# Optimization experiments

Hardware: AMD Instinct MI355X
Metric: run time of the kernel (lower is better)

The kernel has to match this reference:

```python
import jax, jax.numpy as jnp
import numpy as np
import math

VOCAB, D, H, NL, L, B = 50257, 768, 12, 4, 1024, 2
DH = D // H
DFF = 4 * D
ALPHA = 0.25
NEG = -1e9


def _ln(x, g, b, eps=1e-5):
    mu = x.mean(-1, keepdims=True)
    var = ((x - mu) ** 2).mean(-1, keepdims=True)
    return (x - mu) * jax.lax.rsqrt(var + eps) * g + b


def setup_inputs() -> dict:
    key = jax.random.key(0)
    ks = jax.random.split(key, 16)
    s = 0.02
    tokens = jax.random.randint(ks[0], (B, L), 0, VOCAB)
    timelike_mask = jax.random.randint(ks[1], (NL, D), 0, 2).astype(jnp.int32)
    embed = jax.random.normal(ks[2], (VOCAB, D), jnp.float32) * s
    pos_emb = jax.random.normal(ks[3], (L, D), jnp.float32) * s
    wq = jax.random.normal(ks[4], (NL, D, D), jnp.float32) * s
    wk = jax.random.normal(ks[5], (NL, D, D), jnp.float32) * s
    wv = jax.random.normal(ks[6], (NL, D, D), jnp.float32) * s
    wo = jax.random.normal(ks[7], (NL, D, D), jnp.float32) * s
    ff_w1 = jax.random.normal(ks[8], (NL, DFF, D), jnp.float32) * s
    ff_b1 = jnp.zeros((NL, DFF), jnp.float32)
    ff_w2 = jax.random.normal(ks[9], (NL, D, DFF), jnp.float32) * s
    ff_b2 = jnp.zeros((NL, D), jnp.float32)
    ln1_g = jnp.ones((NL, D), jnp.float32); ln1_b = jnp.zeros((NL, D), jnp.float32)
    ln2_g = jnp.ones((NL, D), jnp.float32); ln2_b = jnp.zeros((NL, D), jnp.float32)
    lnf_g = jnp.ones((D,), jnp.float32); lnf_b = jnp.zeros((D,), jnp.float32)
    return dict(tokens=tokens, timelike_mask=timelike_mask, embed=embed, pos_emb=pos_emb,
                wq=wq, wk=wk, wv=wv, wo=wo,
                ln1_g=ln1_g, ln1_b=ln1_b, ln2_g=ln2_g, ln2_b=ln2_b,
                ff_w1=ff_w1, ff_b1=ff_b1, ff_w2=ff_w2, ff_b2=ff_b2,
                lnf_g=lnf_g, lnf_b=lnf_b)


def reference(tokens, timelike_mask, embed, pos_emb, wq, wk, wv, wo,
              ln1_g, ln1_b, ln2_g, ln2_b, ff_w1, ff_b1, ff_w2, ff_b2,
              lnf_g, lnf_b):
    Bc, Lc = tokens.shape
    scale = math.sqrt(DH)
    # embeddings: token + learned position
    h = embed[tokens] + pos_emb[None, :Lc]  # (B,L,D)
    # additive causal mask, matching torch's -inf attention_mask convention
    causal = jnp.where(jnp.tril(jnp.ones((Lc, Lc), bool)), 0.0, NEG)[None, None]  # (1,1,L,L)
    for i in range(NL):
        xn = _ln(h, ln1_g[i], ln1_b[i])
        # nn.Linear(bias=False): y = x @ W.T, W is (out,in)
        q = jnp.einsum('bld,od->blo', xn, wq[i]).reshape(Bc, Lc, H, DH).astype(jnp.float32)
        k = jnp.einsum('bld,od->blo', xn, wk[i]).reshape(Bc, Lc, H, DH).astype(jnp.float32)
        v = jnp.einsum('bld,od->blo', xn, wv[i]).reshape(Bc, Lc, H, DH)
        # Minkowski term: scores_std - 2*alpha*(Q*P_t)K^T  ==  (Q*(1-2*alpha*m)) K^T
        m = timelike_mask[i].astype(jnp.float32).reshape(H, DH)  # per-head timelike directions
        q_eff = q * (1.0 - 2.0 * ALPHA * m)[None, None]
        scores = jnp.einsum('bqhd,bkhd->bhqk', q_eff, k) / scale + causal
        aw = jax.nn.softmax(scores, axis=-1)  # dropout=0 (eval)
        attn = jnp.einsum('bhqk,bkhd->bqhd', aw, v).reshape(Bc, Lc, D)
        h = h + jnp.einsum('bld,od->blo', attn, wo[i])
        xn2 = _ln(h, ln2_g[i], ln2_b[i])
        ff = jax.nn.gelu(jnp.einsum('bld,fd->blf', xn2, ff_w1[i]) + ff_b1[i], approximate=False)
        h = h + jnp.einsum('blf,df->bld', ff, ff_w2[i]) + ff_b2[i]
    h = _ln(h, lnf_g, lnf_b)
    logits = jnp.einsum('bld,vd->blv', h, embed)  # tied LM head
    return logits
```

## Files before the change

kernel.cpp:

```cpp
#include <hip/hip_runtime.h>
#include <math.h>

#define VOCABSZ 50257
#define VPAD 50432
#define DMODEL 768
#define NHEAD 12
#define NLAYER 4
#define SEQ 1024
#define BATCH 2
#define DHEAD 64
#define DFFN 3072
#define BT (BATCH * SEQ)
#define NBH (BATCH * NHEAD)

typedef __attribute__((ext_vector_type(8))) short bf16x8;
typedef __attribute__((ext_vector_type(4))) float f32x4;

__device__ __forceinline__ ushort f2bf(float f) {
  uint u = __builtin_bit_cast(uint, f);
  u = (u + 0x7fffu + ((u >> 16) & 1u)) >> 16;
  return (ushort)u;
}

__device__ __forceinline__ float bf2f(ushort u) {
  uint x = ((uint)u) << 16;
  return __builtin_bit_cast(float, x);
}

__device__ __forceinline__ void gl_lds16(const ushort* g, ushort* l) {
  __builtin_amdgcn_global_load_lds(
      (const __attribute__((address_space(1))) void*)g,
      (__attribute__((address_space(3))) void*)l, 16, 0, 0);
}

__global__ __launch_bounds__(256) void conv_qkv3_kernel(
    const float* __restrict__ wq, const float* __restrict__ wk,
    const float* __restrict__ wv, ushort* __restrict__ dst) {
  const int per4 = DMODEL * DMODEL / 4;
  const int total = NLAYER * per4;
  int i = blockIdx.x * 256 + threadIdx.x;
  if (i >= 3 * total) return;
  int which = i / total;
  int rem = i - which * total;
  const float* src = (which == 0) ? wq : (which == 1) ? wk : wv;
  int layer = rem / per4, r2 = rem % per4;
  float4 v = reinterpret_cast<const float4*>(src)[rem];
  reinterpret_cast<ushort4*>(dst)[(size_t)layer * (3 * per4) + which * per4 +
                                  r2] =
      make_ushort4(f2bf(v.x), f2bf(v.y), f2bf(v.z), f2bf(v.w));
}

__global__ __launch_bounds__(256) void conv3_kernel(
    const float* __restrict__ wo, ushort* __restrict__ wo_b,
    const float* __restrict__ fw1, ushort* __restrict__ fw1_b,
    const float* __restrict__ fw2, ushort* __restrict__ fw2_b) {
  const int n1 = NLAYER * DMODEL * DMODEL / 4;
  const int nf = NLAYER * DFFN * DMODEL / 4;
  int i = blockIdx.x * 256 + threadIdx.x;
  const float* src;
  ushort* dst;
  int idx;
  if (i < n1) {
    src = wo; dst = wo_b; idx = i;
  } else if (i < n1 + nf) {
    src = fw1; dst = fw1_b; idx = i - n1;
  } else if (i < n1 + 2 * nf) {
    src = fw2; dst = fw2_b; idx = i - n1 - nf;
  } else {
    return;
  }
  float4 v = reinterpret_cast<const float4*>(src)[idx];
  reinterpret_cast<ushort4*>(dst)[idx] =
      make_ushort4(f2bf(v.x), f2bf(v.y), f2bf(v.z), f2bf(v.w));
}

__global__ __launch_bounds__(256) void conv_embed_kernel(
    const float* __restrict__ emb, ushort* __restrict__ dst) {
  int i = blockIdx.x * 256 + threadIdx.x;
  if (i >= VPAD * DMODEL / 4) return;
  int row = (i * 4) / DMODEL;
  ushort4 o = make_ushort4(0, 0, 0, 0);
  if (row < VOCABSZ) {
    float4 v = reinterpret_cast<const float4*>(emb)[i];
    o = make_ushort4(f2bf(v.x), f2bf(v.y), f2bf(v.z), f2bf(v.w));
  }
  reinterpret_cast<ushort4*>(dst)[i] = o;
}

template <int KS, bool RBIAS, bool EMB>
__global__ __launch_bounds__(256) void ln_kernel(
    float* __restrict__ h, const ushort* __restrict__ part,
    const float* __restrict__ rb, const int* __restrict__ tok,
    const float* __restrict__ emb, const float* __restrict__ pos,
    const float* __restrict__ g, const float* __restrict__ bta,
    ushort* __restrict__ o) {
  __shared__ float red[8];
  int row = blockIdx.x;
  int tid = threadIdx.x;
  float* xr = h + (size_t)row * DMODEL;
  const float* er = nullptr;
  const float* pr = nullptr;
  if (EMB) {
    er = emb + (size_t)tok[row] * DMODEL;
    pr = pos + (size_t)(row & (SEQ - 1)) * DMODEL;
  }
  float v[3];
  float s = 0.f, sq = 0.f;
#pragma unroll
  for (int j = 0; j < 3; ++j) {
    int c = tid + j * 256;
    float a;
    if (EMB) {
      a = er[c] + pr[c];
      xr[c] = a;
    } else {
      a = xr[c];
      if (RBIAS) a += rb[c];
      if (KS > 0) {
#pragma unroll
        for (int z = 0; z < KS; ++z)
          a += bf2f(part[(size_t)z * BT * DMODEL + (size_t)row * DMODEL + c]);
        xr[c] = a;
      }
    }
    v[j] = a;
    s += a;
    sq += a * a;
  }
#pragma unroll
  for (int off = 1; off < 64; off <<= 1) {
    s += __shfl_xor(s, off);
    sq += __shfl_xor(sq, off);
  }
  int wid = tid >> 6;
  if ((tid & 63) == 0) { red[wid * 2] = s; red[wid * 2 + 1] = sq; }
  __syncthreads();
  float S = red[0] + red[2] + red[4] + red[6];
  float SQ = red[1] + red[3] + red[5] + red[7];
  float mu = S * (1.0f / DMODEL);
  float var = SQ * (1.0f / DMODEL) - mu * mu;
  float r = rsqrtf(var + 1e-5f);
  ushort* orow = o + (size_t)row * DMODEL;
#pragma unroll
  for (int j = 0; j < 3; ++j) {
    int c = tid + j * 256;
    orow[c] = f2bf((v[j] - mu) * r * g[c] + bta[c]);
  }
}

__global__ __launch_bounds__(256) void fattn_kernel(
    const ushort* __restrict__ q, const ushort* __restrict__ k,
    const ushort* __restrict__ vt, float* __restrict__ Opart,
    float* __restrict__ ml) {
  __shared__ __align__(16) ushort Ks[2][64 * 64];
  __shared__ __align__(16) ushort Vs[2][64 * 64];
  __shared__ __align__(16) ushort Ps[4][16][80];
  const int bid = blockIdx.x;
  const int wgid = (bid & 7) * 96 + (bid >> 3);
  const int z = wgid / 32;
  const int rem = wgid % 32;
  const int qb_ = rem >> 1, s = rem & 1;
  const int b = z / NHEAD, hh = z % NHEAD;
  const int q0 = (15 - qb_) * 64;
  const int tcnt = (q0 >> 6) + 1;
  const int half0 = (tcnt + 1) >> 1;
  const int tbeg = s ? half0 : 0;
  const int tend = s ? tcnt : half0;
  const int tid = threadIdx.x, w = tid >> 6, l = tid & 63;
  const int fr = l & 15, ks = l >> 4;
  const int qrow = q0 + w * 16 + fr;
  const size_t ri = (size_t)z * SEQ + qrow;
  const size_t R = (size_t)NBH * SEQ;
  const size_t off = (s ? R : 0) + ri;

  if (tbeg >= tend) {
    f32x4 zero = {};
#pragma unroll
    for (int db = 0; db < 4; ++db)
      *reinterpret_cast<f32x4*>(Opart + off * 64 + db * 16 + ks * 4) = zero;
    if (ks == 0) { ml[off * 2] = -1e30f; ml[off * 2 + 1] = 0.f; }
    return;
  }

  const ushort* qp = q + (size_t)(b * SEQ + qrow) * DMODEL + hh * DHEAD;
  const bf16x8 qf0 = *reinterpret_cast<const bf16x8*>(qp + ks * 8);
  const bf16x8 qf1 = *reinterpret_cast<const bf16x8*>(qp + 32 + ks * 8);

  const int srow = w * 16 + (l >> 3);
  const int g0 = ((l & 7) ^ (srow & 7)) * 8;

  auto stage = [&](int k0, int d) {
#pragma unroll
    for (int c = 0; c < 2; ++c) {
      int r = srow + c * 8;
      gl_lds16(k + (size_t)(b * SEQ + k0 + r) * DMODEL + hh * DHEAD + g0,
               &Ks[d][(w * 16 + c * 8) * 64]);
      gl_lds16(vt + (size_t)(z * 64 + r) * SEQ + k0 + g0,
               &Vs[d][(w * 16 + c * 8) * 64]);
    }
  };

  f32x4 acc_o[4] = {};
  float mrun = -1e30f, lrun = 0.f;

  stage(tbeg * 64, 0);
  for (int t = tbeg; t < tend; ++t) {
    const int cur = (t - tbeg) & 1;
    if (t + 1 < tend) {
      stage((t + 1) * 64, cur ^ 1);
      asm volatile("s_waitcnt vmcnt(4)" ::: "memory");
    } else {
      asm volatile("s_waitcnt vmcnt(0)" ::: "memory");
    }
    __builtin_amdgcn_s_barrier();
    __builtin_amdgcn_sched_barrier(0);
    f32x4 acc_s[4] = {};
#pragma unroll
    for (int kstep = 0; kstep < 2; ++kstep) {
      const bf16x8 qf = kstep ? qf1 : qf0;
#pragma unroll
      for (int kb = 0; kb < 4; ++kb) {
        int ra = kb * 16 + fr;
        bf16x8 af = *reinterpret_cast<const bf16x8*>(
            &Ks[cur][ra * 64 + (((kstep * 4 + ks) ^ (ra & 7)) * 8)]);
        acc_s[kb] =
            __builtin_amdgcn_mfma_f32_16x16x32_bf16(af, qf, acc_s[kb], 0, 0, 0);
      }
    }
    const bool diag = (t == tcnt - 1);
    float pm = -1e30f;
    float sv[4][4];
#pragma unroll
    for (int kb = 0; kb < 4; ++kb)
#pragma unroll
      for (int r = 0; r < 4; ++r) {
        float sc = acc_s[kb][r];
        if (diag && (t * 64 + kb * 16 + ks * 4 + r > qrow)) sc = -1e30f;
        sv[kb][r] = sc;
        pm = fmaxf(pm, sc);
      }
    pm = fmaxf(pm, __shfl_xor(pm, 16));
    pm = fmaxf(pm, __shfl_xor(pm, 32));
    if (!__all(pm - mrun <= 8.0f)) {
      float mnew = fmaxf(mrun, pm);
      float scale = __expf(mrun - mnew);
      lrun *= scale;
#pragma unroll
      for (int db = 0; db < 4; ++db) acc_o[db] *= scale;
      mrun = mnew;
    }
    float psum = 0.f;
#pragma unroll
    for (int kb = 0; kb < 4; ++kb) {
      float p0 = __expf(sv[kb][0] - mrun);
      float p1 = __expf(sv[kb][1] - mrun);
      float p2 = __expf(sv[kb][2] - mrun);
      float p3 = __expf(sv[kb][3] - mrun);
      psum += (p0 + p1) + (p2 + p3);
      *reinterpret_cast<ushort4*>(&Ps[w][fr][kb * 16 + ks * 4]) =
          make_ushort4(f2bf(p0), f2bf(p1), f2bf(p2), f2bf(p3));
    }
    psum += __shfl_xor(psum, 16);
    psum += __shfl_xor(psum, 32);
    lrun += psum;
#pragma unroll
    for (int kstep = 0; kstep < 2; ++kstep) {
      bf16x8 pf =
          *reinterpret_cast<const bf16x8*>(&Ps[w][fr][kstep * 32 + ks * 8]);
#pragma unroll
      for (int db = 0; db < 4; ++db) {
        int rd = db * 16 + fr;
        bf16x8 vf = *reinterpret_cast<const bf16x8*>(
            &Vs[cur][rd * 64 + (((kstep * 4 + ks) ^ (rd & 7)) * 8)]);
        acc_o[db] =
            __builtin_amdgcn_mfma_f32_16x16x32_bf16(vf, pf, acc_o[db], 0, 0, 0);
      }
    }
    __builtin_amdgcn_sched_barrier(0);
    __builtin_amdgcn_s_barrier();
  }
#pragma unroll
  for (int db = 0; db < 4; ++db)
    *reinterpret_cast<f32x4*>(Opart + off * 64 + db * 16 + ks * 4) = acc_o[db];
  if (ks == 0) { ml[off * 2] = mrun; ml[off * 2 + 1] = lrun; }
}

__global__ __launch_bounds__(256) void fmerge_kernel(
    const float* __restrict__ Opart, const float* __restrict__ ml,
    ushort* __restrict__ o) {
  int ri = blockIdx.x * 4 + (threadIdx.x >> 6);
  int d = threadIdx.x & 63;
  int z = ri >> 10, qrow = ri & (SEQ - 1);
  int b = z / NHEAD, hh = z % NHEAD;
  const size_t R = (size_t)NBH * SEQ;
  float m0 = ml[(size_t)ri * 2], l0 = ml[(size_t)ri * 2 + 1];
  float m1 = ml[(R + ri) * 2], l1 = ml[(R + ri) * 2 + 1];
  float M = fmaxf(m0, m1);
  float e0 = __expf(m0 - M), e1 = __expf(m1 - M);
  float L = l0 * e0 + l1 * e1;
  float v0 = Opart[(size_t)ri * 64 + d];
  float v1 = Opart[(R + ri) * 64 + d];
  float v = (v0 * e0 + v1 * e1) / L;
  o[(size_t)(b * SEQ + qrow) * DMODEL + hh * DHEAD + d] = f2bf(v);
}

template <bool QKV, bool BIAS, bool GELU, bool RES, bool OUTBF, bool SWZ,
          bool PART>
__global__ __launch_bounds__(256) void gemm_bf16_nt(
    const ushort* __restrict__ A, const ushort* __restrict__ B,
    const float* __restrict__ bias, const int* __restrict__ tmask,
    const float* __restrict__ res, float* __restrict__ Cf,
    ushort* __restrict__ Cb, int ldc, ushort* __restrict__ qb,
    ushort* __restrict__ kb, ushort* __restrict__ vt, int M, int K, int Nreal,
    int kchunk) {
  __shared__ __align__(16) ushort As[2][128 * 32];
  __shared__ __align__(16) ushort Bs[2][128 * 32];
  int bnx, bmy;
  if (SWZ) {
    int bid = blockIdx.x;
    int chunk = gridDim.x >> 3;
    int wgid = (bid & 7) * chunk + (bid >> 3);
    int mb = M >> 7;
    bmy = wgid % mb;
    bnx = wgid / mb;
  } else {
    bnx = blockIdx.x;
    bmy = blockIdx.y;
  }
  const int m0 = bmy * 128, n0 = bnx * 128;
  const int kbeg = PART ? blockIdx.z * kchunk : 0;
  const int kend = PART ? kbeg + kchunk : K;
  if (PART) Cb += (size_t)blockIdx.z * M * ldc;
  const int tid = threadIdx.x;
  const int w = tid >> 6, l = tid & 63;
  const int wr = w >> 1, wc = w & 1;
  const int fr = l & 15, ks = l >> 4;

  const int seg0 = w * 2, seg1 = w * 2 + 1;
  const int srow0 = seg0 * 16 + (l >> 2);
  const int srow1 = seg1 * 16 + (l >> 2);
  const int koff0 = (((l & 3) ^ ((srow0 >> 1) & 3))) * 8;
  const int koff1 = (((l & 3) ^ ((srow1 >> 1) & 3))) * 8;
  const ushort* A0 = A + (size_t)(m0 + srow0) * K + koff0;
  const ushort* A1 = A + (size_t)(m0 + srow1) * K + koff1;
  const ushort* B0 = B + (size_t)(n0 + srow0) * K + koff0;
  const ushort* B1 = B + (size_t)(n0 + srow1) * K + koff1;

  int aoff[4], boff[4];
#pragma unroll
  for (int i = 0; i < 4; ++i) {
    int ra = wr * 64 + i * 16 + fr;
    aoff[i] = ra * 32 + ((ks ^ ((ra >> 1) & 3)) * 8);
    int rb = wc * 64 + i * 16 + fr;
    boff[i] = rb * 32 + ((ks ^ ((rb >> 1) & 3)) * 8);
  }

  gl_lds16(A0 + kbeg, &As[0][seg0 * 512]);
  gl_lds16(A1 + kbeg, &As[0][seg1 * 512]);
  gl_lds16(B0 + kbeg, &Bs[0][seg0 * 512]);
  gl_lds16(B1 + kbeg, &Bs[0][seg1 * 512]);

  f32x4 acc[4][4] = {};
  int cur = 0;
  for (int k0 = kbeg; k0 < kend; k0 += 32) {
    const int nxt = k0 + 32;
    if (nxt < kend) {
      gl_lds16(A0 + nxt, &As[cur ^ 1][seg0 * 512]);
      gl_lds16(A1 + nxt, &As[cur ^ 1][seg1 * 512]);
      gl_lds16(B0 + nxt, &Bs[cur ^ 1][seg0 * 512]);
      gl_lds16(B1 + nxt, &Bs[cur ^ 1][seg1 * 512]);
      asm volatile("s_waitcnt vmcnt(4)" ::: "memory");
    } else {
      asm volatile("s_waitcnt vmcnt(0)" ::: "memory");
    }
    __builtin_amdgcn_s_barrier();
    __builtin_amdgcn_sched_barrier(0);
    bf16x8 af[4], bfr[4];
#pragma unroll
    for (int i = 0; i < 4; ++i)
      af[i] = *reinterpret_cast<const bf16x8*>(&As[cur][aoff[i]]);
#pragma unroll
    for (int i = 0; i < 4; ++i)
      bfr[i] = *reinterpret_cast<const bf16x8*>(&Bs[cur][boff[i]]);
#pragma unroll
    for (int mi = 0; mi < 4; ++mi)
#pragma unroll
      for (int nj = 0; nj < 4; ++nj)
        acc[mi][nj] = __builtin_amdgcn_mfma_f32_16x16x32_bf16(
            af[mi], bfr[nj], acc[mi][nj], 0, 0, 0);
    __builtin_amdgcn_sched_barrier(0);
    __builtin_amdgcn_s_barrier();
    cur ^= 1;
  }

#pragma unroll
  for (int mi = 0; mi < 4; ++mi) {
#pragma unroll
    for (int nj = 0; nj < 4; ++nj) {
      int n = n0 + wc * 64 + nj * 16 + fr;
      if (n < Nreal) {
        if (PART) {
#pragma unroll
          for (int r = 0; r < 4; ++r) {
            int m = m0 + wr * 64 + mi * 16 + ks * 4 + r;
            Cb[(size_t)m * ldc + n] = f2bf(acc[mi][nj][r]);
          }
        } else if (QKV) {
          if (n < DMODEL) {
            float sc = (1.0f - 0.5f * (float)tmask[n]) * 0.125f;
#pragma unroll
            for (int r = 0; r < 4; ++r) {
              int m = m0 + wr * 64 + mi * 16 + ks * 4 + r;
              qb[(size_t)m * DMODEL + n] = f2bf(acc[mi][nj][r] * sc);
            }
          } else if (n < 2 * DMODEL) {
#pragma unroll
            for (int r = 0; r < 4; ++r) {
              int m = m0 + wr * 64 + mi * 16 + ks * 4 + r;
              kb[(size_t)m * DMODEL + (n - DMODEL)] = f2bf(acc[mi][nj][r]);
            }
          } else {
            int d = n - 2 * DMODEL;
            int key = (m0 & (SEQ - 1)) + wr * 64 + mi * 16 + ks * 4;
            size_t zr = (size_t)((m0 >> 10) * NHEAD + (d >> 6)) * 64 + (d & 63);
            ushort4 p4 = make_ushort4(
                f2bf(acc[mi][nj][0]), f2bf(acc[mi][nj][1]),
                f2bf(acc[mi][nj][2]), f2bf(acc[mi][nj][3]));
            *reinterpret_cast<ushort4*>(vt + zr * SEQ + key) = p4;
          }
        } else {
#pragma unroll
          for (int r = 0; r < 4; ++r) {
            int m = m0 + wr * 64 + mi * 16 + ks * 4 + r;
            float v = acc[mi][nj][r];
            if (BIAS) v += bias[n];
            if (GELU) v = 0.5f * v * (1.0f + erff(v * 0.70710678118f));
            if (RES) v += res[(size_t)m * ldc + n];
            if (OUTBF)
              Cb[(size_t)m * ldc + n] = f2bf(v);
            else
              Cf[(size_t)m * ldc + n] = v;
          }
        }
      }
    }
  }
}

__global__ __launch_bounds__(512, 2) void gemm_lmhead(
    const ushort* __restrict__ A, const ushort* __restrict__ B,
    float* __restrict__ C) {
  __shared__ __align__(16) ushort SMEM[4 * 256 * 64];
  const int K = DMODEL;
  const int NTILE = K / 64;
  const int ITERS = NTILE / 2;

  const int bid = blockIdx.x;
  const int chunk = gridDim.x >> 3;
  const int wgid = (bid & 7) * chunk + (bid >> 3);
  const int m0 = (wgid & 7) * 256;
  const int n0 = (wgid >> 3) * 256;

  const int tid = threadIdx.x;
  const int w = tid >> 6, l = tid & 63;
  const int wr = w >> 2, wc = w & 3;
  const int fr = l & 15, ks = l >> 4;

  const int strow = tid >> 3;
  const int stk = ((tid & 7) ^ (strow & 7)) * 8;
  const int wseg = (w << 3) * 64;

  const int fsw0 = (ks ^ (fr & 7)) * 8;
  const int fsw1 = ((4 | ks) ^ (fr & 7)) * 8;
  const int arow = (wr * 128 + fr) * 64;
  const int brow = (wc * 64 + fr) * 64;

  bf16x8 Ar[4][2], Br[4][2];
  f32x4 acc[8][4] = {};

#define STA(d, kt, rb)                                            \
  gl_lds16(A + (size_t)(m0 + (rb) + strow) * K + (kt) * 64 + stk, \
           SMEM + (d) * 16384 + (rb) * 64 + wseg)
#define STB(d, kt, rb)                                            \
  gl_lds16(B + (size_t)(n0 + (rb) + strow) * K + (kt) * 64 + stk, \
           SMEM + 32768 + (d) * 16384 + (rb) * 64 + wseg)
#define RDA(d, mi, kst)                           \
  (*reinterpret_cast<const bf16x8*>(              \
      &SMEM[(d) * 16384 + arow + (mi) * 1024 + ((kst) ? fsw1 : fsw0)]))
#define RDB(d, nj, kst)                           \
  (*reinterpret_cast<const bf16x8*>(              \
      &SMEM[32768 + (d) * 16384 + brow + (nj) * 1024 + ((kst) ? fsw1 : fsw0)]))
#define MMAQ(mh, nh)                                                       \
  _Pragma("unroll") for (int kst = 0; kst < 2; ++kst)                      \
  _Pragma("unroll") for (int mi = 0; mi < 4; ++mi)                         \
  _Pragma("unroll") for (int nj = 0; nj < 2; ++nj)                         \
    acc[(mh)*4 + mi][(nh)*2 + nj] = __builtin_amdgcn_mfma_f32_16x16x32_bf16( \
        Ar[mi][kst], Br[(nh)*2 + nj][kst], acc[(mh)*4 + mi][(nh)*2 + nj],  \
        0, 0, 0)
#define BAR __builtin_amdgcn_s_barrier()
#define PRIO1 __builtin_amdgcn_s_setprio(1)
#define PRIO0 __builtin_amdgcn_s_setprio(0)

  STA(0, 0, 0); STA(0, 0, 64); STA(0, 0, 128); STA(0, 0, 192);
  STB(0, 0, 0); STB(0, 0, 64); STB(0, 0, 128); STB(0, 0, 192);
  STB(1, 1, 0); STB(1, 1, 64); STB(1, 1, 128); STB(1, 1, 192);
  asm volatile("s_waitcnt vmcnt(4)" ::: "memory");
  BAR;

  for (int it = 0; it < ITERS; ++it) {
    const int t1 = 2 * it + 1;
    const int tn = 2 * it + 2;
    const bool s0 = tn < NTILE, s1 = tn + 1 < NTILE;
#pragma unroll
    for (int mi = 0; mi < 4; ++mi) {
      Ar[mi][0] = RDA(0, mi, 0); Ar[mi][1] = RDA(0, mi, 1);
    }
#pragma unroll
    for (int nj = 0; nj < 2; ++nj) {
      Br[nj][0] = RDB(0, nj, 0); Br[nj][1] = RDB(0, nj, 1);
    }
    STA(1, t1, 0); STA(1, t1, 64);
    BAR; PRIO1; MMAQ(0, 0); PRIO0; BAR;
#pragma unroll
    for (int nj = 2; nj < 4; ++nj) {
      Br[nj][0] = RDB(0, nj, 0); Br[nj][1] = RDB(0, nj, 1);
    }
    STA(1, t1, 128); STA(1, t1, 192);
    BAR; PRIO1; MMAQ(0, 1); PRIO0; BAR;
#pragma unroll
    for (int mi = 0; mi < 4; ++mi) {
      Ar[mi][0] = RDA(0, mi + 4, 0); Ar[mi][1] = RDA(0, mi + 4, 1);
    }
    if (s0) { STB(0, tn, 0); STB(0, tn, 64); }
    BAR; PRIO1; MMAQ(1, 1); PRIO0; BAR;
    if (s0) { STB(0, tn, 128); STB(0, tn, 192); }
    BAR; PRIO1; MMAQ(1, 0); PRIO0;
    if (s0)
      asm volatile("s_waitcnt vmcnt(4)" ::: "memory");
    else
      asm volatile("s_waitcnt vmcnt(0)" ::: "memory");
    BAR;
#pragma unroll
    for (int mi = 0; mi < 4; ++mi) {
      Ar[mi][0] = RDA(1, mi, 0); Ar[mi][1] = RDA(1, mi, 1);
    }
#pragma unroll
    for (int nj = 0; nj < 2; ++nj) {
      Br[nj][0] = RDB(1, nj, 0); Br[nj][1] = RDB(1, nj, 1);
    }
    if (s0) { STA(0, tn, 0); STA(0, tn, 64); }
    BAR; PRIO1; MMAQ(0, 0); PRIO0; BAR;
#pragma unroll
    for (int nj = 2; nj < 4; ++nj) {
      Br[nj][0] = RDB(1, nj, 0); Br[nj][1] = RDB(1, nj, 1);
    }
    if (s0) { STA(0, tn, 128); STA(0, tn, 192); }
    BAR; PRIO1; MMAQ(0, 1); PRIO0; BAR;
#pragma unroll
    for (int mi = 0; mi < 4; ++mi) {
      Ar[mi][0] = RDA(1, mi + 4, 0); Ar[mi][1] = RDA(1, mi + 4, 1);
    }
    if (s1) { STB(1, tn + 1, 0); STB(1, tn + 1, 64); }
    BAR; PRIO1; MMAQ(1, 1); PRIO0; BAR;
    if (s1) { STB(1, tn + 1, 128); STB(1, tn + 1, 192); }
    BAR; PRIO1; MMAQ(1, 0); PRIO0;
    if (it + 1 < ITERS) {
      asm volatile("s_waitcnt vmcnt(4)" ::: "memory");
      BAR;
    }
  }

  float* eb = reinterpret_cast<float*>(SMEM);
#pragma unroll 1
  for (int p = 0; p < 2; ++p) {
    __syncthreads();
    if (wr == p) {
#pragma unroll
      for (int mi = 0; mi < 8; ++mi)
#pragma unroll
        for (int nj = 0; nj < 4; ++nj)
#pragma unroll
          for (int r = 0; r < 4; ++r)
            eb[(mi * 16 + ks * 4 + r) * 256 + wc * 64 + nj * 16 + fr] =
                acc[mi][nj][r];
    }
    __syncthreads();
    const size_t rowbase = (size_t)(m0 + p * 128) * VOCABSZ + n0;
#pragma unroll 8
    for (int c = 0; c < 64; ++c) {
      int lin = c * 512 + tid;
      int row = lin >> 8, col = lin & 255;
      if (n0 + col < VOCABSZ) {
        __builtin_nontemporal_store(
            eb[lin], C + rowbase + (size_t)row * VOCABSZ + col);
      }
    }
  }
#undef STA
#undef STB
#undef RDA
#undef RDB
#undef MMAQ
#undef BAR
#undef PRIO1
#undef PRIO0
}

extern "C" void kernel_launch(void* const* d_in, const int* in_sizes, int n_in,
                              void* d_out, int out_size, void* d_ws,
                              size_t ws_size, hipStream_t stream) {
  const int* tokens = (const int*)d_in[0];
  const int* tmask = (const int*)d_in[1];
  const float* embed = (const float*)d_in[2];
  const float* pos = (const float*)d_in[3];
  const float* wq = (const float*)d_in[4];
  const float* wk = (const float*)d_in[5];
  const float* wv = (const float*)d_in[6];
  const float* wo = (const float*)d_in[7];
  const float* ln1g = (const float*)d_in[8];
  const float* ln1b = (const float*)d_in[9];
  const float* ln2g = (const float*)d_in[10];
  const float* ln2b = (const float*)d_in[11];
  const float* fw1 = (const float*)d_in[12];
  const float* fb1 = (const float*)d_in[13];
  const float* fw2 = (const float*)d_in[14];
  const float* fb2 = (const float*)d_in[15];
  const float* lnfg = (const float*)d_in[16];
  const float* lnfb = (const float*)d_in[17];

  char* wp = (char*)d_ws;
  auto alloc = [&](size_t bytes) {
    void* p = wp;
    wp += (bytes + 255) & ~(size_t)255;
    return p;
  };
  float* h = (float*)alloc((size_t)BT * DMODEL * 4);
  ushort* part = (ushort*)alloc((size_t)8 * BT * DMODEL * 2);
  float* opart = (float*)alloc((size_t)2 * NBH * SEQ * DHEAD * 4);
  float* mlb = (float*)alloc((size_t)2 * NBH * SEQ * 2 * 4);
  ushort* qb = (ushort*)alloc((size_t)BT * DMODEL * 2);
  ushort* kb = (ushort*)alloc((size_t)BT * DMODEL * 2);
  ushort* vt = (ushort*)alloc((size_t)NBH * DHEAD * SEQ * 2);
  ushort* xn = (ushort*)alloc((size_t)BT * DMODEL * 2);
  ushort* ab = (ushort*)alloc((size_t)BT * DMODEL * 2);
  ushort* ffb = (ushort*)alloc((size_t)BT * DFFN * 2);
  ushort* wqkv_b = (ushort*)alloc((size_t)NLAYER * 3 * DMODEL * DMODEL * 2);
  ushort* wo_b = (ushort*)alloc((size_t)NLAYER * DMODEL * DMODEL * 2);
  ushort* fw1_b = (ushort*)alloc((size_t)NLAYER * DFFN * DMODEL * 2);
  ushort* fw2_b = (ushort*)alloc((size_t)NLAYER * DMODEL * DFFN * 2);
  ushort* emb_b = (ushort*)alloc((size_t)VPAD * DMODEL * 2);

  const int per4 = DMODEL * DMODEL / 4;
  const int nff4 = NLAYER * DFFN * DMODEL / 4;
  conv_qkv3_kernel<<<(3 * NLAYER * per4 + 255) / 256, 256, 0, stream>>>(
      wq, wk, wv, wqkv_b);
  conv3_kernel<<<(NLAYER * per4 + 2 * nff4 + 255) / 256, 256, 0, stream>>>(
      wo, wo_b, fw1, fw1_b, fw2, fw2_b);
  conv_embed_kernel<<<(VPAD * DMODEL / 4 + 255) / 256, 256, 0, stream>>>(
      embed, emb_b);

  const dim3 gqkv(3 * DMODEL / 128, BT / 128);
  const dim3 gff(DFFN / 128, BT / 128);
  const dim3 gwo(DMODEL / 128, BT / 128, 4);
  const dim3 gff2(DMODEL / 128, BT / 128, 8);

  for (int i = 0; i < NLAYER; ++i) {
    if (i == 0)
      ln_kernel<0, false, true><<<BT, 256, 0, stream>>>(
          h, nullptr, nullptr, tokens, embed, pos, ln1g, ln1b, xn);
    else
      ln_kernel<8, true, false><<<BT, 256, 0, stream>>>(
          h, part, fb2 + (i - 1) * DMODEL, nullptr, nullptr, nullptr,
          ln1g + i * DMODEL, ln1b + i * DMODEL, xn);

    gemm_bf16_nt<true, false, false, false, false, false, false>
        <<<gqkv, 256, 0, stream>>>(
            xn, wqkv_b + (size_t)i * 3 * DMODEL * DMODEL, nullptr,
            tmask + i * DMODEL, nullptr, nullptr, nullptr, 0, qb, kb, vt, BT,
            DMODEL, 3 * DMODEL, DMODEL);

    fattn_kernel<<<2 * NBH * (SEQ / 64), 256, 0, stream>>>(qb, kb, vt, opart,
                                                           mlb);
    fmerge_kernel<<<NBH * SEQ / 4, 256, 0, stream>>>(opart, mlb, ab);

    gemm_bf16_nt<false, false, false, false, false, false, true>
        <<<gwo, 256, 0, stream>>>(
            ab, wo_b + (size_t)i * DMODEL * DMODEL, nullptr, nullptr, nullptr,
            nullptr, part, DMODEL, nullptr, nullptr, nullptr, BT, DMODEL,
            DMODEL, DMODEL / 4);

    ln_kernel<4, false, false><<<BT, 256, 0, stream>>>(
        h, part, nullptr, nullptr, nullptr, nullptr, ln2g + i * DMODEL,
        ln2b + i * DMODEL, xn);

    gemm_bf16_nt<false, true, true, false, true, false, false>
        <<<gff, 256, 0, stream>>>(
            xn, fw1_b + (size_t)i * DFFN * DMODEL, fb1 + i * DFFN, nullptr,
            nullptr, nullptr, ffb, DFFN, nullptr, nullptr, nullptr, BT, DMODEL,
            DFFN, DMODEL);

    gemm_bf16_nt<false, false, false, false, false, false, true>
        <<<gff2, 256, 0, stream>>>(
            ffb, fw2_b + (size_t)i * DMODEL * DFFN, nullptr, nullptr, nullptr,
            nullptr, part, DMODEL, nullptr, nullptr, nullptr, BT, DFFN, DMODEL,
            DFFN / 8);
  }

  ln_kernel<8, true, false><<<BT, 256, 0, stream>>>(
      h, part, fb2 + (NLAYER - 1) * DMODEL, nullptr, nullptr, nullptr, lnfg,
      lnfb, xn);

  gemm_lmhead<<<8 * (VPAD / 256), 512, 0, stream>>>(xn, emb_b, (float*)d_out);
}
```

Before: 838.1 us.

## Restructure LM-head GEMM to simple double-buffered K=32 pipeline with direct stores

Replaces the hand-interleaved ping-pong LM-head GEMM (K tile 64, quarter-step MFMA/load interleave, LDS-staged coalesced epilogue) with a simpler double-buffered loop over K tiles of 32. Each step issues the next tile's loads, then runs all 32 MFMAs. LDS use is halved and launch bounds now ask for 4 blocks per CU, aiming for more occupancy and less barrier overhead. Output is stored straight from registers, which gives strided, poorly coalesced writes to the large logits array and may raise register pressure.

Result: slower. 1.828 ms (+118.1%).

```diff
diff --git a/kernel.cpp b/kernel.cpp
--- a/kernel.cpp
+++ b/kernel.cpp
@@ -447,13 +447,13 @@
   }
 }
 
-__global__ __launch_bounds__(512, 2) void gemm_lmhead(
+__global__ __launch_bounds__(512, 4) void gemm_lmhead(
     const ushort* __restrict__ A, const ushort* __restrict__ B,
     float* __restrict__ C) {
-  __shared__ __align__(16) ushort SMEM[4 * 256 * 64];
+  __shared__ __align__(16) ushort As[2][256 * 32];
+  __shared__ __align__(16) ushort Bs[2][256 * 32];
   const int K = DMODEL;
-  const int NTILE = K / 64;
-  const int ITERS = NTILE / 2;
+  const int NT = K / 32;
 
   const int bid = blockIdx.x;
   const int chunk = gridDim.x >> 3;
@@ -466,144 +466,76 @@
   const int wr = w >> 2, wc = w & 3;
   const int fr = l & 15, ks = l >> 4;
 
-  const int strow = tid >> 3;
-  const int stk = ((tid & 7) ^ (strow & 7)) * 8;
-  const int wseg = (w << 3) * 64;
-
-  const int fsw0 = (ks ^ (fr & 7)) * 8;
-  const int fsw1 = ((4 | ks) ^ (fr & 7)) * 8;
-  const int arow = (wr * 128 + fr) * 64;
-  const int brow = (wc * 64 + fr) * 64;
-
-  bf16x8 Ar[4][2], Br[4][2];
+  const int koff = ((l & 3) ^ ((l >> 3) & 3)) * 8;
+  const int srw = w * 16 + (l >> 2);
+
+  int aoff[8], boff[4];
+#pragma unroll
+  for (int mi = 0; mi < 8; ++mi) {
+    int ra = wr * 128 + mi * 16 + fr;
+    aoff[mi] = ra * 32 + ((ks ^ ((ra >> 1) & 3)) * 8);
+  }
+#pragma unroll
+  for (int nj = 0; nj < 4; ++nj) {
+    int rb = wc * 64 + nj * 16 + fr;
+    boff[nj] = rb * 32 + ((ks ^ ((rb >> 1) & 3)) * 8);
+  }
+
+  auto stage = [&](int t, int d) {
+#pragma unroll
+    for (int c = 0; c < 2; ++c) {
+      gl_lds16(A + (size_t)(m0 + c * 128 + srw) * K + t * 32 + koff,
+               &As[d][(c * 128 + w * 16) * 32]);
+      gl_lds16(B + (size_t)(n0 + c * 128 + srw) * K + t * 32 + koff,
+               &Bs[d][(c * 128 + w * 16) * 32]);
+    }
+  };
+
   f32x4 acc[8][4] = {};
-
-#define STA(d, kt, rb)                                            \
-  gl_lds16(A + (size_t)(m0 + (rb) + strow) * K + (kt) * 64 + stk, \
-           SMEM + (d) * 16384 + (rb) * 64 + wseg)
-#define STB(d, kt, rb)                                            \
-  gl_lds16(B + (size_t)(n0 + (rb) + strow) * K + (kt) * 64 + stk, \
-           SMEM + 32768 + (d) * 16384 + (rb) * 64 + wseg)
-#define RDA(d, mi, kst)                           \
-  (*reinterpret_cast<const bf16x8*>(              \
-      &SMEM[(d) * 16384 + arow + (mi) * 1024 + ((kst) ? fsw1 : fsw0)]))
-#define RDB(d, nj, kst)                           \
-  (*reinterpret_cast<const bf16x8*>(              \
-      &SMEM[32768 + (d) * 16384 + brow + (nj) * 1024 + ((kst) ? fsw1 : fsw0)]))
-#define MMAQ(mh, nh)                                                       \
-  _Pragma("unroll") for (int kst = 0; kst < 2; ++kst)                      \
-  _Pragma("unroll") for (int mi = 0; mi < 4; ++mi)                         \
-  _Pragma("unroll") for (int nj = 0; nj < 2; ++nj)                         \
-    acc[(mh)*4 + mi][(nh)*2 + nj] = __builtin_amdgcn_mfma_f32_16x16x32_bf16( \
-        Ar[mi][kst], Br[(nh)*2 + nj][kst], acc[(mh)*4 + mi][(nh)*2 + nj],  \
-        0, 0, 0)
-#define BAR __builtin_amdgcn_s_barrier()
-#define PRIO1 __builtin_amdgcn_s_setprio(1)
-#define PRIO0 __builtin_amdgcn_s_setprio(0)
-
-  STA(0, 0, 0); STA(0, 0, 64); STA(0, 0, 128); STA(0, 0, 192);
-  STB(0, 0, 0); STB(0, 0, 64); STB(0, 0, 128); STB(0, 0, 192);
-  STB(1, 1, 0); STB(1, 1, 64); STB(1, 1, 128); STB(1, 1, 192);
-  asm volatile("s_waitcnt vmcnt(4)" ::: "memory");
-  BAR;
-
-  for (int it = 0; it < ITERS; ++it) {
-    const int t1 = 2 * it + 1;
-    const int tn = 2 * it + 2;
-    const bool s0 = tn < NTILE, s1 = tn + 1 < NTILE;
-#pragma unroll
-    for (int mi = 0; mi < 4; ++mi) {
-      Ar[mi][0] = RDA(0, mi, 0); Ar[mi][1] = RDA(0, mi, 1);
-    }
-#pragma unroll
-    for (int nj = 0; nj < 2; ++nj) {
-      Br[nj][0] = RDB(0, nj, 0); Br[nj][1] = RDB(0, nj, 1);
-    }
-    STA(1, t1, 0); STA(1, t1, 64);
-    BAR; PRIO1; MMAQ(0, 0); PRIO0; BAR;
-#pragma unroll
-    for (int nj = 2; nj < 4; ++nj) {
-      Br[nj][0] = RDB(0, nj, 0); Br[nj][1] = RDB(0, nj, 1);
-    }
-    STA(1, t1, 128); STA(1, t1, 192);
-    BAR; PRIO1; MMAQ(0, 1); PRIO0; BAR;
-#pragma unroll
-    for (int mi = 0; mi < 4; ++mi) {
-      Ar[mi][0] = RDA(0, mi + 4, 0); Ar[mi][1] = RDA(0, mi + 4, 1);
-    }
-    if (s0) { STB(0, tn, 0); STB(0, tn, 64); }
-    BAR; PRIO1; MMAQ(1, 1); PRIO0; BAR;
-    if (s0) { STB(0, tn, 128); STB(0, tn, 192); }
-    BAR; PRIO1; MMAQ(1, 0); PRIO0;
-    if (s0)
+  stage(0, 0);
+  int cur = 0;
+  for (int t = 0; t < NT; ++t) {
+    if (t + 1 < NT) {
+      stage(t + 1, cur ^ 1);
       asm volatile("s_waitcnt vmcnt(4)" ::: "memory");
-    else
+    } else {
       asm volatile("s_waitcnt vmcnt(0)" ::: "memory");
-    BAR;
-#pragma unroll
-    for (int mi = 0; mi < 4; ++mi) {
-      Ar[mi][0] = RDA(1, mi, 0); Ar[mi][1] = RDA(1, mi, 1);
-    }
-#pragma unroll
-    for (int nj = 0; nj < 2; ++nj) {
-      Br[nj][0] = RDB(1, nj, 0); Br[nj][1] = RDB(1, nj, 1);
-    }
-    if (s0) { STA(0, tn, 0); STA(0, tn, 64); }
-    BAR; PRIO1; MMAQ(0, 0); PRIO0; BAR;
-#pragma unroll
-    for (int nj = 2; nj < 4; ++nj) {
-      Br[nj][0] = RDB(1, nj, 0); Br[nj][1] = RDB(1, nj, 1);
-    }
-    if (s0) { STA(0, tn, 128); STA(0, tn, 192); }
-    BAR; PRIO1; MMAQ(0, 1); PRIO0; BAR;
-#pragma unroll
-    for (int mi = 0; mi < 4; ++mi) {
-      Ar[mi][0] = RDA(1, mi + 4, 0); Ar[mi][1] = RDA(1, mi + 4, 1);
-    }
-    if (s1) { STB(1, tn + 1, 0); STB(1, tn + 1, 64); }
-    BAR; PRIO1; MMAQ(1, 1); PRIO0; BAR;
-    if (s1) { STB(1, tn + 1, 128); STB(1, tn + 1, 192); }
-    BAR; PRIO1; MMAQ(1, 0); PRIO0;
-    if (it + 1 < ITERS) {
-      asm volatile("s_waitcnt vmcnt(4)" ::: "memory");
-      BAR;
-    }
-  }
-
-  float* eb = reinterpret_cast<float*>(SMEM);
-#pragma unroll 1
-  for (int p = 0; p < 2; ++p) {
-    __syncthreads();
-    if (wr == p) {
-#pragma unroll
-      for (int mi = 0; mi < 8; ++mi)
-#pragma unroll
-        for (int nj = 0; nj < 4; ++nj)
-#pragma unroll
-          for (int r = 0; r < 4; ++r)
-            eb[(mi * 16 + ks * 4 + r) * 256 + wc * 64 + nj * 16 + fr] =
-                acc[mi][nj][r];
-    }
-    __syncthreads();
-    const size_t rowbase = (size_t)(m0 + p * 128) * VOCABSZ + n0;
-#pragma unroll 8
-    for (int c = 0; c < 64; ++c) {
-      int lin = c * 512 + tid;
-      int row = lin >> 8, col = lin & 255;
-      if (n0 + col < VOCABSZ) {
-        __builtin_nontemporal_store(
-            eb[lin], C + rowbase + (size_t)row * VOCABSZ + col);
+    }
+    __builtin_amdgcn_s_barrier();
+    __builtin_amdgcn_sched_barrier(0);
+    bf16x8 bfr[4];
+#pragma unroll
+    for (int nj = 0; nj < 4; ++nj)
+      bfr[nj] = *reinterpret_cast<const bf16x8*>(&Bs[cur][boff[nj]]);
+    __builtin_amdgcn_s_setprio(1);
+#pragma unroll
+    for (int mi = 0; mi < 8; ++mi) {
+      bf16x8 af = *reinterpret_cast<const bf16x8*>(&As[cur][aoff[mi]]);
+#pragma unroll
+      for (int nj = 0; nj < 4; ++nj)
+        acc[mi][nj] = __builtin_amdgcn_mfma_f32_16x16x32_bf16(
+            af, bfr[nj], acc[mi][nj], 0, 0, 0);
+    }
+    __builtin_amdgcn_s_setprio(0);
+    __builtin_amdgcn_sched_barrier(0);
+    __builtin_amdgcn_s_barrier();
+    cur ^= 1;
+  }
+
+#pragma unroll
+  for (int mi = 0; mi < 8; ++mi) {
+#pragma unroll
+    for (int nj = 0; nj < 4; ++nj) {
+      int n = n0 + wc * 64 + nj * 16 + fr;
+      if (n < VOCABSZ) {
+        int m = m0 + wr * 128 + mi * 16 + ks * 4;
+#pragma unroll
+        for (int r = 0; r < 4; ++r)
+          __builtin_nontemporal_store(acc[mi][nj][r],
+                                      C + (size_t)(m + r) * VOCABSZ + n);
       }
     }
   }
-#undef STA
-#undef STB
-#undef RDA
-#undef RDB
-#undef MMAQ
-#undef BAR
-#undef PRIO1
-#undef PRIO0
 }
 
 extern "C" void kernel_launch(void* const* d_in, const int* in_sizes, int n_in,
```
